# Kernel optimization log

Hardware: AMD Instinct MI355X
Metric: run time of the kernel (lower is better)

The kernel has to match this reference:

```python
import jax, jax.numpy as jnp
import numpy as np

B, T, EPROJS, DUNITS, ATT_DIM = 32, 2048, 512, 512, 512
ACONV_CHANS, ACONV_FILT = 32, 100
SCALING = 2.0


def _lin(k, fan_in, fan_out):
    k1, k2 = jax.random.split(k)
    lim = 1.0 / np.sqrt(fan_in)
    w = jax.random.uniform(k1, (fan_in, fan_out), minval=-lim, maxval=lim, dtype=jnp.float32)
    b = jax.random.uniform(k2, (fan_out,), minval=-lim, maxval=lim, dtype=jnp.float32)
    return w, b


def setup_inputs() -> dict:
    key = jax.random.key(0)
    ks = jax.random.split(key, 16)
    W_w, W_b = _lin(ks[0], DUNITS, ATT_DIM)
    V_w, V_b = _lin(ks[1], EPROJS, ATT_DIM)
    U_w, U_b = _lin(ks[2], DUNITS, ATT_DIM)
    g_w, g_b = _lin(ks[3], ATT_DIM, 1)
    K = 2 * ACONV_FILT + 1
    lim = 1.0 / np.sqrt(K)
    conv_w = jax.random.uniform(ks[4], (ACONV_CHANS, 1, K), minval=-lim, maxval=lim, dtype=jnp.float32)
    lim = 1.0 / np.sqrt(ATT_DIM)
    W_ih = jax.random.uniform(ks[5], (4 * ATT_DIM, ACONV_CHANS), minval=-lim, maxval=lim, dtype=jnp.float32)
    W_hh = jax.random.uniform(ks[6], (4 * ATT_DIM, ATT_DIM), minval=-lim, maxval=lim, dtype=jnp.float32)
    b_ih = jax.random.uniform(ks[7], (4 * ATT_DIM,), minval=-lim, maxval=lim, dtype=jnp.float32)
    b_hh = jax.random.uniform(ks[8], (4 * ATT_DIM,), minval=-lim, maxval=lim, dtype=jnp.float32)
    enc_hs_pad = jax.random.normal(ks[9], (B, T, EPROJS), dtype=jnp.float32)
    enc_hs_len = jax.random.randint(ks[10], (B,), T // 2, T + 1, dtype=jnp.int32)
    dec_z = jax.random.normal(ks[11], (B, DUNITS), dtype=jnp.float32)
    att_prev = jax.random.uniform(ks[12], (B, T), dtype=jnp.float32)
    att_h = jax.random.normal(ks[13], (B, ATT_DIM), dtype=jnp.float32)
    att_c = jax.random.normal(ks[14], (B, ATT_DIM), dtype=jnp.float32)
    return dict(enc_hs_pad=enc_hs_pad, enc_hs_len=enc_hs_len, dec_z=dec_z,
                att_prev=att_prev, att_h=att_h, att_c=att_c,
                W_w=W_w, W_b=W_b, V_w=V_w, V_b=V_b, U_w=U_w, U_b=U_b,
                g_w=g_w, g_b=g_b, conv_w=conv_w,
                W_ih=W_ih, W_hh=W_hh, b_ih=b_ih, b_hh=b_hh)


def reference(enc_hs_pad, enc_hs_len, dec_z, att_prev, att_h, att_c,
              W_w, W_b, V_w, V_b, U_w, U_b, g_w, g_b, conv_w,
              W_ih, W_hh, b_ih, b_hh):
    # pre-computed encoder projection: (B, T, att_dim)
    pre = jnp.einsum('bte,ea->bta', enc_hs_pad, V_w) + V_b
    # location conv over previous attention weights: (B, C, T)
    conv = jax.lax.conv_general_dilated(att_prev[:, None, :], conv_w,
                                        window_strides=(1,),
                                        padding=[(ACONV_FILT, ACONV_FILT)],
                                        dimension_numbers=('NCH', 'OIH', 'NCH'))
    feat = jnp.max(jax.nn.relu(conv), axis=-1)  # (B, C): max-pool over time
    # LSTMCell (torch gate order: i, f, g, o)
    gates = feat @ W_ih.T + b_ih + att_h @ W_hh.T + b_hh
    i, f, g, o = jnp.split(gates, 4, axis=-1)
    c_new = jax.nn.sigmoid(f) * att_c + jax.nn.sigmoid(i) * jnp.tanh(g)
    h_new = jax.nn.sigmoid(o) * jnp.tanh(c_new)
    # additive score
    dec_proj = dec_z @ U_w + U_b            # (B, att_dim)
    wh = h_new @ W_w + W_b                  # (B, att_dim)
    e = jnp.tanh(wh[:, None, :] + pre + dec_proj[:, None, :])  # (B, T, att_dim)
    score = jnp.einsum('bta,a->bt', e, g_w[:, 0]) + g_b[0]     # (B, T)
    mask = jnp.arange(T)[None, :] >= enc_hs_len[:, None]
    score = jnp.where(mask, jnp.asarray(-1e30, score.dtype), score)
    w = jax.nn.softmax(SCALING * score, axis=1)
    c_v = jnp.einsum('bte,bt->be', enc_hs_pad, w)  # (B, eprojs)
    return c_v, w, h_new, c_new
```

## Files before the change

kernel.cpp:

```cpp
#include <hip/hip_runtime.h>
#include <math.h>

#define BB 32
#define TT_SEQ 2048
#define EPROJS 512
#define ATT 512
#define NCH 32
#define FILT 100
#define KCONV 201
#define G4 2048

typedef unsigned short ushort_t;
typedef unsigned int uint_t;
typedef __attribute__((ext_vector_type(8))) short bf16x8_t;
typedef __attribute__((ext_vector_type(4))) float f32x4_t;

__device__ inline ushort_t f2bf(float f) {
    uint_t u = __float_as_uint(f);
    uint_t r = (u + 0x7fffu + ((u >> 16) & 1u)) >> 16;
    return (ushort_t)r;
}

__device__ inline float tanh_fast(float x) {
    float e = __expf(2.0f * x);
    return 1.0f - 2.0f / (e + 1.0f);
}

__global__ __launch_bounds__(256) void k_pre(const float* __restrict__ att_prev,
                                             const float* __restrict__ conv_w,
                                             float* __restrict__ feat,
                                             const float* __restrict__ vw,
                                             ushort_t* __restrict__ vwt,
                                             const float* __restrict__ U_b,
                                             const float* __restrict__ W_b,
                                             const float* __restrict__ V_b,
                                             float* __restrict__ add_vec) {
    __shared__ __align__(16) float shbuf[64 * 65];
    __shared__ float red[4];
    if (blockIdx.x < 1024) {
        int b = blockIdx.x >> 5;
        int c = blockIdx.x & 31;
        float* row = shbuf;
        for (int i = threadIdx.x; i < TT_SEQ + 2 * FILT + 8; i += 256) {
            int t = i - FILT;
            row[i] = (t >= 0 && t < TT_SEQ) ? att_prev[b * TT_SEQ + t] : 0.0f;
        }
        __syncthreads();
        const float* cw = conv_w + c * KCONV;
        int t0 = threadIdx.x * 8;
        float acc[8] = {0.f, 0.f, 0.f, 0.f, 0.f, 0.f, 0.f, 0.f};
        float4 r0 = *(const float4*)(row + t0);
        float4 r1 = *(const float4*)(row + t0 + 4);
        float r[8] = {r0.x, r0.y, r0.z, r0.w, r1.x, r1.y, r1.z, r1.w};
        for (int k = 0; k < 200; k += 8) {
            float4 n0 = *(const float4*)(row + t0 + k + 8);
            float4 n1 = *(const float4*)(row + t0 + k + 12);
            float nn[8] = {n0.x, n0.y, n0.z, n0.w, n1.x, n1.y, n1.z, n1.w};
            #pragma unroll
            for (int kk = 0; kk < 8; ++kk) {
                float w = cw[k + kk];
                #pragma unroll
                for (int i = 0; i < 8; ++i) {
                    float rv = (kk + i < 8) ? r[kk + i] : nn[kk + i - 8];
                    acc[i] = fmaf(w, rv, acc[i]);
                }
            }
            #pragma unroll
            for (int i = 0; i < 8; ++i) r[i] = nn[i];
        }
        float wlast = cw[200];
        #pragma unroll
        for (int i = 0; i < 8; ++i) acc[i] = fmaf(wlast, r[i], acc[i]);
        float m = 0.0f;
        #pragma unroll
        for (int i = 0; i < 8; ++i) m = fmaxf(m, acc[i]);
        #pragma unroll
        for (int off = 32; off; off >>= 1) m = fmaxf(m, __shfl_xor(m, off, 64));
        if ((threadIdx.x & 63) == 0) red[threadIdx.x >> 6] = m;
        __syncthreads();
        if (threadIdx.x == 0) {
            m = fmaxf(fmaxf(red[0], red[1]), fmaxf(red[2], red[3]));
            feat[b * NCH + c] = m;
        }
    } else {
        int id = blockIdx.x - 1024;
        int eb = (id & 7) * 64, ab = (id >> 3) * 64;
        float (*tile)[65] = (float (*)[65])shbuf;
        for (int it = 0; it < 16; ++it) {
            int idx = threadIdx.x + it * 256;
            int r = idx >> 6, c = idx & 63;
            tile[r][c] = vw[(size_t)(eb + r) * ATT + ab + c];
        }
        __syncthreads();
        for (int it = 0; it < 16; ++it) {
            int idx = threadIdx.x + it * 256;
            int r = idx >> 6, c = idx & 63;
            vwt[(size_t)(ab + r) * EPROJS + eb + c] = f2bf(tile[c][r]);
        }
        int i = id * 256 + threadIdx.x;
        int a = i & 511;
        add_vec[i] = U_b[a] + W_b[a] + V_b[a];
    }
}

#define HP 518
__global__ __launch_bounds__(256) void k_gates(const float* __restrict__ feat,
                                               const float* __restrict__ att_h,
                                               const float* __restrict__ W_ih,
                                               const float* __restrict__ W_hh,
                                               const float* __restrict__ b_ih,
                                               const float* __restrict__ b_hh,
                                               float* __restrict__ gates) {
    __shared__ float hsh[32 * HP];
    __shared__ float fsh[32 * 33];
    int tid = threadIdx.x;
    for (int i = tid; i < 32 * 512; i += 256) {
        int r = i >> 9, c = i & 511;
        hsh[r * HP + c] = att_h[i];
    }
    for (int i = tid; i < 1024; i += 256) fsh[(i >> 5) * 33 + (i & 31)] = feat[i];
    __syncthreads();
    int jl = tid >> 5, b = tid & 31;
    int j = blockIdx.x * 8 + jl;
    float acc = b_ih[j] + b_hh[j];
    const float4* wi = (const float4*)(W_ih + (size_t)j * NCH);
    #pragma unroll
    for (int k4 = 0; k4 < 8; ++k4) {
        float4 w = wi[k4];
        const float* f = fsh + b * 33 + k4 * 4;
        acc = fmaf(w.x, f[0], acc);
        acc = fmaf(w.y, f[1], acc);
        acc = fmaf(w.z, f[2], acc);
        acc = fmaf(w.w, f[3], acc);
    }
    const float4* wh = (const float4*)(W_hh + (size_t)j * ATT);
    float a0 = 0.f, a1 = 0.f, a2 = 0.f, a3 = 0.f;
    #pragma unroll 8
    for (int k4 = 0; k4 < 128; ++k4) {
        float4 w = wh[k4];
        float2 h0 = *(const float2*)(hsh + b * HP + k4 * 4);
        float2 h1 = *(const float2*)(hsh + b * HP + k4 * 4 + 2);
        a0 = fmaf(w.x, h0.x, a0);
        a1 = fmaf(w.y, h0.y, a1);
        a2 = fmaf(w.z, h1.x, a2);
        a3 = fmaf(w.w, h1.y, a3);
    }
    gates[(size_t)b * G4 + j] = acc + ((a0 + a1) + (a2 + a3));
}

__global__ __launch_bounds__(256) void k_hz(const float* __restrict__ gates,
                                            const float* __restrict__ att_c,
                                            const float* __restrict__ dec_z,
                                            const float* __restrict__ U_w,
                                            const float* __restrict__ W_w,
                                            float* __restrict__ h_out,
                                            float* __restrict__ c_out,
                                            float* __restrict__ add_vec) {
    int a0 = blockIdx.x * 32;
    int k0 = blockIdx.y * 64;
    __shared__ float zsh[32 * 65];
    __shared__ float hsh[32 * 65];
    __shared__ float us[64 * 33];
    __shared__ float ws2[64 * 33];
    int tid = threadIdx.x;
    for (int i = tid; i < 2048; i += 256) {
        int b = i >> 6, d = i & 63;
        int idx = b * ATT + k0 + d;
        const float* g = gates + (size_t)b * G4 + k0 + d;
        float ig = g[0], fg = g[ATT], gg = g[2 * ATT], og = g[3 * ATT];
        float si = 1.0f / (1.0f + expf(-ig));
        float sf = 1.0f / (1.0f + expf(-fg));
        float so = 1.0f / (1.0f + expf(-og));
        float cn = sf * att_c[idx] + si * tanhf(gg);
        float hn = so * tanhf(cn);
        hsh[b * 65 + d] = hn;
        if (blockIdx.x == 0) { c_out[idx] = cn; h_out[idx] = hn; }
        zsh[b * 65 + d] = dec_z[idx];
        int dr = i >> 5, c = i & 31;
        us[dr * 33 + c] = U_w[(size_t)(k0 + dr) * ATT + a0 + c];
        ws2[dr * 33 + c] = W_w[(size_t)(k0 + dr) * ATT + a0 + c];
    }
    __syncthreads();
    int al = tid >> 5, b = tid & 31;
    float acc[4] = {0.f, 0.f, 0.f, 0.f};
    for (int d = 0; d < 64; ++d) {
        float zv = zsh[b * 65 + d];
        float hv = hsh[b * 65 + d];
        #pragma unroll
        for (int m = 0; m < 4; ++m) {
            int a = al + 8 * m;
            acc[m] = fmaf(zv, us[d * 33 + a], acc[m]);
            acc[m] = fmaf(hv, ws2[d * 33 + a], acc[m]);
        }
    }
    #pragma unroll
    for (int m = 0; m < 4; ++m)
        atomicAdd(&add_vec[(size_t)b * ATT + a0 + al + 8 * m], acc[m]);
}

__global__ __launch_bounds__(512, 2) void k_gemm_score2(
        const float* __restrict__ enc,
        const ushort_t* __restrict__ Btbf,
        const float* __restrict__ add_vec,
        const float* __restrict__ g_w,
        const int* __restrict__ lens,
        float* __restrict__ score) {
    int mtile = blockIdx.x;
    int b = mtile >> 4;
    int t0 = (mtile & 15) * 128;
    if (t0 >= lens[b]) return;

    __shared__ __align__(16) ushort_t sA[128 * 64];
    __shared__ __align__(16) ushort_t sB[512 * 64];

    int tid = threadIdx.x;
    int lane = tid & 63;
    int wave = tid >> 6;
    int wm = wave >> 2, wn = wave & 3;
    int q = lane >> 4, l15 = lane & 15;

    const float* Ag = enc + (size_t)mtile * 128 * EPROJS;

    f32x4_t acc[4][8];
    #pragma unroll
    for (int i = 0; i < 4; ++i)
        #pragma unroll
        for (int j = 0; j < 8; ++j) acc[i][j] = (f32x4_t){0.f, 0.f, 0.f, 0.f};

    for (int kc = 0; kc < 8; ++kc) {
        __syncthreads();
        #pragma unroll
        for (int it = 0; it < 8; ++it) {
            int g = tid + it * 512;
            int n = g >> 3;
            int kq = g & 7;
            int kqs = kq ^ (n & 7);
            __builtin_amdgcn_global_load_lds(
                (const __attribute__((address_space(1))) void*)(Btbf + (size_t)n * EPROJS + kc * 64 + kqs * 8),
                (__attribute__((address_space(3))) void*)(sB + g * 8), 16, 0, 0);
        }
        #pragma unroll
        for (int it = 0; it < 2; ++it) {
            int g = tid + it * 512;
            int m = g >> 3;
            int kq = g & 7;
            int kqs = kq ^ (m & 7);
            const float* src = Ag + (size_t)m * EPROJS + kc * 64 + kqs * 8;
            float4 v0 = *(const float4*)(src);
            float4 v1 = *(const float4*)(src + 4);
            bf16x8_t o;
            o[0] = (short)f2bf(v0.x); o[1] = (short)f2bf(v0.y);
            o[2] = (short)f2bf(v0.z); o[3] = (short)f2bf(v0.w);
            o[4] = (short)f2bf(v1.x); o[5] = (short)f2bf(v1.y);
            o[6] = (short)f2bf(v1.z); o[7] = (short)f2bf(v1.w);
            *(bf16x8_t*)(sA + g * 8) = o;
        }
        __syncthreads();
        #pragma unroll
        for (int s = 0; s < 2; ++s) {
            bf16x8_t af[4], bfr[8];
            int kq = s * 4 + q;
            #pragma unroll
            for (int i = 0; i < 4; ++i) {
                int m = wm * 64 + i * 16 + l15;
                af[i] = *(const bf16x8_t*)(sA + (m * 8 + (kq ^ (m & 7))) * 8);
            }
            #pragma unroll
            for (int j = 0; j < 8; ++j) {
                int n = wn * 128 + j * 16 + l15;
                bfr[j] = *(const bf16x8_t*)(sB + (n * 8 + (kq ^ (n & 7))) * 8);
            }
            #pragma unroll
            for (int i = 0; i < 4; ++i)
                #pragma unroll
                for (int j = 0; j < 8; ++j)
                    acc[i][j] = __builtin_amdgcn_mfma_f32_16x16x32_bf16(af[i], bfr[j], acc[i][j], 0, 0, 0);
        }
    }

    float g8[8], av8[8];
    #pragma unroll
    for (int j = 0; j < 8; ++j) {
        int a = wn * 128 + j * 16 + l15;
        g8[j] = g_w[a];
        av8[j] = add_vec[b * ATT + a];
    }
    float s_ir[4][4];
    #pragma unroll
    for (int i = 0; i < 4; ++i) {
        #pragma unroll
        for (int r = 0; r < 4; ++r) {
            float s = 0.0f;
            #pragma unroll
            for (int j = 0; j < 8; ++j) {
                float x = acc[i][j][r] + av8[j];
                s = fmaf(g8[j], tanh_fast(x), s);
            }
            s_ir[i][r] = s;
        }
    }
    #pragma unroll
    for (int off = 8; off; off >>= 1) {
        #pragma unroll
        for (int i = 0; i < 4; ++i)
            #pragma unroll
            for (int r = 0; r < 4; ++r)
                s_ir[i][r] += __shfl_xor(s_ir[i][r], off, 16);
    }
    __syncthreads();
    float* sred = (float*)sA;
    if (tid < 128) sred[tid] = 0.0f;
    __syncthreads();
    if (l15 == 0) {
        #pragma unroll
        for (int i = 0; i < 4; ++i)
            #pragma unroll
            for (int r = 0; r < 4; ++r)
                atomicAdd(&sred[wm * 64 + i * 16 + q * 4 + r], s_ir[i][r]);
    }
    __syncthreads();
    if (tid < 128) score[b * TT_SEQ + t0 + tid] = sred[tid];
}

__global__ __launch_bounds__(256) void k_softmax(const float* __restrict__ score,
                                                 const int* __restrict__ lens,
                                                 float* __restrict__ w_out,
                                                 float* __restrict__ c_v) {
    int b = blockIdx.x;
    int len = lens[b];
    __shared__ float red[4];
    float vals[8];
    float m = -INFINITY;
    #pragma unroll
    for (int i = 0; i < 8; ++i) {
        int t = threadIdx.x + i * 256;
        float s = (t < len) ? 2.0f * score[b * TT_SEQ + t] : -INFINITY;
        vals[i] = s;
        m = fmaxf(m, s);
    }
    #pragma unroll
    for (int off = 32; off; off >>= 1) m = fmaxf(m, __shfl_xor(m, off, 64));
    if ((threadIdx.x & 63) == 0) red[threadIdx.x >> 6] = m;
    __syncthreads();
    m = fmaxf(fmaxf(red[0], red[1]), fmaxf(red[2], red[3]));
    __syncthreads();
    float sum = 0.0f;
    #pragma unroll
    for (int i = 0; i < 8; ++i) {
        float e = expf(vals[i] - m);
        vals[i] = e;
        sum += e;
    }
    #pragma unroll
    for (int off = 32; off; off >>= 1) sum += __shfl_xor(sum, off, 64);
    if ((threadIdx.x & 63) == 0) red[threadIdx.x >> 6] = sum;
    __syncthreads();
    sum = red[0] + red[1] + red[2] + red[3];
    float inv = 1.0f / sum;
    #pragma unroll
    for (int i = 0; i < 8; ++i) w_out[b * TT_SEQ + threadIdx.x + i * 256] = vals[i] * inv;
    for (int i = threadIdx.x; i < EPROJS; i += 256) c_v[b * EPROJS + i] = 0.0f;
}

__global__ __launch_bounds__(256) void k_ctx64(const float* __restrict__ enc,
                                               const float* __restrict__ w,
                                               const int* __restrict__ lens,
                                               float* __restrict__ c_v) {
    int b = blockIdx.y;
    int t0 = blockIdx.x * 64;
    if (t0 >= lens[b]) return;
    __shared__ float wsh[64];
    if (threadIdx.x < 64) wsh[threadIdx.x] = w[b * TT_SEQ + t0 + threadIdx.x];
    __syncthreads();
    const float* base = enc + ((size_t)b * TT_SEQ + t0) * EPROJS;
    float a0 = 0.f, a1 = 0.f;
    for (int t = 0; t < 64; ++t) {
        float wt = wsh[t];
        a0 = fmaf(wt, base[(size_t)t * EPROJS + threadIdx.x], a0);
        a1 = fmaf(wt, base[(size_t)t * EPROJS + threadIdx.x + 256], a1);
    }
    atomicAdd(&c_v[b * EPROJS + threadIdx.x], a0);
    atomicAdd(&c_v[b * EPROJS + threadIdx.x + 256], a1);
}

__global__ __launch_bounds__(256) void k_conv_fb(const float* __restrict__ att_prev,
                                                 const float* __restrict__ conv_w,
                                                 float* __restrict__ feat) {
    int b = blockIdx.x >> 5;
    int c = blockIdx.x & 31;
    __shared__ float row[TT_SEQ + 2 * FILT];
    __shared__ float wsh[KCONV];
    __shared__ float red[4];
    for (int i = threadIdx.x; i < TT_SEQ + 2 * FILT; i += 256) {
        int t = i - FILT;
        row[i] = (t >= 0 && t < TT_SEQ) ? att_prev[b * TT_SEQ + t] : 0.0f;
    }
    for (int i = threadIdx.x; i < KCONV; i += 256) wsh[i] = conv_w[c * KCONV + i];
    __syncthreads();
    float m = 0.0f;
    for (int t = threadIdx.x; t < TT_SEQ; t += 256) {
        float s = 0.0f;
        #pragma unroll 4
        for (int k = 0; k < KCONV; ++k) s = fmaf(wsh[k], row[t + k], s);
        m = fmaxf(m, s);
    }
    #pragma unroll
    for (int off = 32; off; off >>= 1) m = fmaxf(m, __shfl_xor(m, off, 64));
    if ((threadIdx.x & 63) == 0) red[threadIdx.x >> 6] = m;
    __syncthreads();
    if (threadIdx.x == 0) {
        m = fmaxf(fmaxf(red[0], red[1]), fmaxf(red[2], red[3]));
        feat[b * NCH + c] = m;
    }
}

__global__ __launch_bounds__(256) void k_lstm(const float* __restrict__ feat,
                                              const float* __restrict__ att_h,
                                              const float* __restrict__ att_c,
                                              const float* __restrict__ W_ih,
                                              const float* __restrict__ W_hh,
                                              const float* __restrict__ b_ih,
                                              const float* __restrict__ b_hh,
                                              float* __restrict__ h_out,
                                              float* __restrict__ c_out) {
    int b = blockIdx.x;
    __shared__ float fsh[NCH];
    __shared__ float hsh[ATT];
    __shared__ float gsh[G4];
    if (threadIdx.x < NCH) fsh[threadIdx.x] = feat[b * NCH + threadIdx.x];
    for (int i = threadIdx.x; i < ATT; i += 256) hsh[i] = att_h[b * ATT + i];
    __syncthreads();
    for (int j = threadIdx.x; j < G4; j += 256) {
        float acc = b_ih[j] + b_hh[j];
        const float* wi = W_ih + (size_t)j * NCH;
        #pragma unroll
        for (int c = 0; c < NCH; ++c) acc = fmaf(fsh[c], wi[c], acc);
        const float* wh = W_hh + (size_t)j * ATT;
        for (int a = 0; a < ATT; a += 4) {
            float4 w4 = *(const float4*)(wh + a);
            acc = fmaf(hsh[a + 0], w4.x, acc);
            acc = fmaf(hsh[a + 1], w4.y, acc);
            acc = fmaf(hsh[a + 2], w4.z, acc);
            acc = fmaf(hsh[a + 3], w4.w, acc);
        }
        gsh[j] = acc;
    }
    __syncthreads();
    for (int a = threadIdx.x; a < ATT; a += 256) {
        float ig = gsh[a], fg = gsh[ATT + a], gg = gsh[2 * ATT + a], og = gsh[3 * ATT + a];
        float si = 1.0f / (1.0f + expf(-ig));
        float sf = 1.0f / (1.0f + expf(-fg));
        float so = 1.0f / (1.0f + expf(-og));
        float cn = sf * att_c[b * ATT + a] + si * tanhf(gg);
        float hn = so * tanhf(cn);
        c_out[b * ATT + a] = cn;
        h_out[b * ATT + a] = hn;
    }
}

__global__ __launch_bounds__(256) void k_addvec(const float* __restrict__ dec_z,
                                                const float* __restrict__ h_new,
                                                const float* __restrict__ U_w,
                                                const float* __restrict__ U_b,
                                                const float* __restrict__ W_w,
                                                const float* __restrict__ W_b,
                                                const float* __restrict__ V_b,
                                                float* __restrict__ add_vec) {
    int b = blockIdx.x;
    __shared__ float zsh[ATT];
    __shared__ float hsh[ATT];
    for (int i = threadIdx.x; i < ATT; i += 256) {
        zsh[i] = dec_z[b * ATT + i];
        hsh[i] = h_new[b * ATT + i];
    }
    __syncthreads();
    for (int a = threadIdx.x; a < ATT; a += 256) {
        float acc = U_b[a] + W_b[a] + V_b[a];
        for (int d = 0; d < ATT; ++d) {
            acc = fmaf(zsh[d], U_w[(size_t)d * ATT + a], acc);
            acc = fmaf(hsh[d], W_w[(size_t)d * ATT + a], acc);
        }
        add_vec[b * ATT + a] = acc;
    }
}

#define TTILE 16
#define SR 516
__global__ __launch_bounds__(256) void k_score(const float* __restrict__ enc,
                                               const float* __restrict__ V_w,
                                               const float* __restrict__ add_vec,
                                               const float* __restrict__ g_w,
                                               const float* __restrict__ g_b,
                                               const int* __restrict__ lens,
                                               float* __restrict__ score) {
    int b = blockIdx.y;
    int t0 = blockIdx.x * TTILE;
    int len = lens[b];
    if (t0 >= len) return;
    __shared__ float enc_t[TTILE * SR];
    __shared__ float ash[ATT];
    __shared__ float gwsh[ATT];
    const float* src = enc + ((size_t)b * TT_SEQ + t0) * EPROJS;
    for (int i = threadIdx.x; i < TTILE * 128; i += 256) {
        int r = i >> 7, c4 = (i & 127) << 2;
        *(float4*)(enc_t + r * SR + c4) = *(const float4*)(src + (size_t)r * EPROJS + c4);
    }
    for (int i = threadIdx.x; i < ATT; i += 256) {
        ash[i] = add_vec[b * ATT + i];
        gwsh[i] = g_w[i];
    }
    __syncthreads();
    int t = threadIdx.x >> 4;
    int al = threadIdx.x & 15;
    const float* er = enc_t + t * SR;
    float sc = 0.0f;
    #pragma unroll
    for (int c = 0; c < 2; ++c) {
        float4 acc0 = {0, 0, 0, 0}, acc1 = {0, 0, 0, 0}, acc2 = {0, 0, 0, 0}, acc3 = {0, 0, 0, 0};
        int abase = c * 256 + al * 4;
        const float* vp = V_w + abase;
        for (int e = 0; e < EPROJS; ++e) {
            float s = er[e];
            const float* rowp = vp + (size_t)e * ATT;
            float4 w0 = *(const float4*)(rowp);
            float4 w1 = *(const float4*)(rowp + 64);
            float4 w2 = *(const float4*)(rowp + 128);
            float4 w3 = *(const float4*)(rowp + 192);
            acc0.x = fmaf(s, w0.x, acc0.x); acc0.y = fmaf(s, w0.y, acc0.y);
            acc0.z = fmaf(s, w0.z, acc0.z); acc0.w = fmaf(s, w0.w, acc0.w);
            acc1.x = fmaf(s, w1.x, acc1.x); acc1.y = fmaf(s, w1.y, acc1.y);
            acc1.z = fmaf(s, w1.z, acc1.z); acc1.w = fmaf(s, w1.w, acc1.w);
            acc2.x = fmaf(s, w2.x, acc2.x); acc2.y = fmaf(s, w2.y, acc2.y);
            acc2.z = fmaf(s, w2.z, acc2.z); acc2.w = fmaf(s, w2.w, acc2.w);
            acc3.x = fmaf(s, w3.x, acc3.x); acc3.y = fmaf(s, w3.y, acc3.y);
            acc3.z = fmaf(s, w3.z, acc3.z); acc3.w = fmaf(s, w3.w, acc3.w);
        }
        float av[16] = {acc0.x, acc0.y, acc0.z, acc0.w,
                        acc1.x, acc1.y, acc1.z, acc1.w,
                        acc2.x, acc2.y, acc2.z, acc2.w,
                        acc3.x, acc3.y, acc3.z, acc3.w};
        #pragma unroll
        for (int k = 0; k < 16; ++k) {
            int a = abase + (k >> 2) * 64 + (k & 3);
            sc = fmaf(gwsh[a], tanhf(av[k] + ash[a]), sc);
        }
    }
    #pragma unroll
    for (int off = 8; off; off >>= 1) sc += __shfl_xor(sc, off, 16);
    if (al == 0) score[b * TT_SEQ + t0 + t] = sc + g_b[0];
}

extern "C" void kernel_launch(void* const* d_in, const int* in_sizes, int n_in,
                              void* d_out, int out_size, void* d_ws, size_t ws_size,
                              hipStream_t stream) {
    const float* enc      = (const float*)d_in[0];
    const int*   lens     = (const int*)d_in[1];
    const float* dec_z    = (const float*)d_in[2];
    const float* att_prev = (const float*)d_in[3];
    const float* att_h    = (const float*)d_in[4];
    const float* att_c    = (const float*)d_in[5];
    const float* W_w      = (const float*)d_in[6];
    const float* W_b      = (const float*)d_in[7];
    const float* V_w      = (const float*)d_in[8];
    const float* V_b      = (const float*)d_in[9];
    const float* U_w      = (const float*)d_in[10];
    const float* U_b      = (const float*)d_in[11];
    const float* g_w      = (const float*)d_in[12];
    const float* g_b      = (const float*)d_in[13];
    const float* conv_w   = (const float*)d_in[14];
    const float* W_ih     = (const float*)d_in[15];
    const float* W_hh     = (const float*)d_in[16];
    const float* b_ih     = (const float*)d_in[17];
    const float* b_hh     = (const float*)d_in[18];

    float* out   = (float*)d_out;
    float* c_v   = out;
    float* w_out = out + BB * EPROJS;
    float* h_out = w_out + BB * TT_SEQ;
    float* c_out = h_out + BB * ATT;

    const size_t need = (size_t)ATT * EPROJS * 2 +
                        (size_t)(1024 + BB * ATT + BB * TT_SEQ + BB * G4) * sizeof(float);

    if (ws_size >= need) {
        ushort_t* vwt  = (ushort_t*)d_ws;
        float* feat    = (float*)(vwt + (size_t)ATT * EPROJS);
        float* add_vec = feat + 1024;
        float* score   = add_vec + BB * ATT;
        float* gates   = score + BB * TT_SEQ;

        k_pre<<<dim3(1024 + 64), dim3(256), 0, stream>>>(att_prev, conv_w, feat,
                                                         V_w, vwt, U_b, W_b, V_b, add_vec);
        k_gates<<<dim3(G4 / 8), dim3(256), 0, stream>>>(feat, att_h, W_ih, W_hh,
                                                        b_ih, b_hh, gates);
        k_hz<<<dim3(16, 8), dim3(256), 0, stream>>>(gates, att_c, dec_z, U_w, W_w,
                                                    h_out, c_out, add_vec);
        k_gemm_score2<<<dim3(512), dim3(512), 0, stream>>>(enc, vwt, add_vec, g_w,
                                                           lens, score);
        k_softmax<<<dim3(BB), dim3(256), 0, stream>>>(score, lens, w_out, c_v);
        k_ctx64<<<dim3(32, BB), dim3(256), 0, stream>>>(enc, w_out, lens, c_v);
    } else {
        float* ws      = (float*)d_ws;
        float* feat    = ws;
        float* add_vec = ws + 1024;
        float* score   = ws + 1024 + BB * ATT;

        k_conv_fb<<<dim3(BB * NCH), dim3(256), 0, stream>>>(att_prev, conv_w, feat);
        k_lstm<<<dim3(BB), dim3(256), 0, stream>>>(feat, att_h, att_c, W_ih, W_hh,
                                                   b_ih, b_hh, h_out, c_out);
        k_addvec<<<dim3(BB), dim3(256), 0, stream>>>(dec_z, h_out, U_w, U_b, W_w, W_b,
                                                     V_b, add_vec);
        k_score<<<dim3(TT_SEQ / TTILE, BB), dim3(256), 0, stream>>>(enc, V_w, add_vec,
                                                                    g_w, g_b, lens, score);
        k_softmax<<<dim3(BB), dim3(256), 0, stream>>>(score, lens, w_out, c_v);
        k_ctx64<<<dim3(32, BB), dim3(256), 0, stream>>>(enc, w_out, lens, c_v);
    }
}
```

Before: 326.5 us.

## Split score GEMM across attention-dim tiles and reduce scores atomically

```diff
diff --git a/kernel.cpp b/kernel.cpp
--- a/kernel.cpp
+++ b/kernel.cpp
@@ -34,7 +34,8 @@
                                              const float* __restrict__ U_b,
                                              const float* __restrict__ W_b,
                                              const float* __restrict__ V_b,
-                                             float* __restrict__ add_vec) {
+                                             float* __restrict__ add_vec,
+                                             float* __restrict__ score) {
     __shared__ __align__(16) float shbuf[64 * 65];
     __shared__ float red[4];
     if (blockIdx.x < 1024) {
@@ -100,6 +101,7 @@
         int i = id * 256 + threadIdx.x;
         int a = i & 511;
         add_vec[i] = U_b[a] + W_b[a] + V_b[a];
+        ((float4*)score)[id * 256 + threadIdx.x] = (float4){0.f, 0.f, 0.f, 0.f};
     }
 }
 
@@ -198,7 +200,7 @@
         atomicAdd(&add_vec[(size_t)b * ATT + a0 + al + 8 * m], acc[m]);
 }
 
-__global__ __launch_bounds__(512, 2) void k_gemm_score2(
+__global__ __launch_bounds__(256) void k_gemm_score3(
         const float* __restrict__ enc,
         const ushort_t* __restrict__ Btbf,
         const float* __restrict__ add_vec,
@@ -209,39 +211,44 @@
     int b = mtile >> 4;
     int t0 = (mtile & 15) * 128;
     if (t0 >= lens[b]) return;
+    int n0 = blockIdx.y * 128;
 
     __shared__ __align__(16) ushort_t sA[128 * 64];
-    __shared__ __align__(16) ushort_t sB[512 * 64];
+    __shared__ __align__(16) ushort_t sB[128 * 64];
+    __shared__ float sred[128];
 
     int tid = threadIdx.x;
     int lane = tid & 63;
     int wave = tid >> 6;
-    int wm = wave >> 2, wn = wave & 3;
+    int wm = wave >> 1, wn = wave & 1;
     int q = lane >> 4, l15 = lane & 15;
 
+    if (tid < 128) sred[tid] = 0.0f;
+
     const float* Ag = enc + (size_t)mtile * 128 * EPROJS;
-
-    f32x4_t acc[4][8];
+    const ushort_t* Bg = Btbf + (size_t)n0 * EPROJS;
+
+    f32x4_t acc[4][4];
     #pragma unroll
     for (int i = 0; i < 4; ++i)
         #pragma unroll
-        for (int j = 0; j < 8; ++j) acc[i][j] = (f32x4_t){0.f, 0.f, 0.f, 0.f};
+        for (int j = 0; j < 4; ++j) acc[i][j] = (f32x4_t){0.f, 0.f, 0.f, 0.f};
 
     for (int kc = 0; kc < 8; ++kc) {
         __syncthreads();
         #pragma unroll
-        for (int it = 0; it < 8; ++it) {
-            int g = tid + it * 512;
+        for (int it = 0; it < 4; ++it) {
+            int g = tid + it * 256;
             int n = g >> 3;
             int kq = g & 7;
             int kqs = kq ^ (n & 7);
             __builtin_amdgcn_global_load_lds(
-                (const __attribute__((address_space(1))) void*)(Btbf + (size_t)n * EPROJS + kc * 64 + kqs * 8),
+                (const __attribute__((address_space(1))) void*)(Bg + (size_t)n * EPROJS + kc * 64 + kqs * 8),
                 (__attribute__((address_space(3))) void*)(sB + g * 8), 16, 0, 0);
         }
         #pragma unroll
-        for (int it = 0; it < 2; ++it) {
-            int g = tid + it * 512;
+        for (int it = 0; it < 4; ++it) {
+            int g = tid + it * 256;
             int m = g >> 3;
             int kq = g & 7;
             int kqs = kq ^ (m & 7);
@@ -258,7 +265,7 @@
         __syncthreads();
         #pragma unroll
         for (int s = 0; s < 2; ++s) {
-            bf16x8_t af[4], bfr[8];
+            bf16x8_t af[4], bfr[4];
             int kq = s * 4 + q;
             #pragma unroll
             for (int i = 0; i < 4; ++i) {
@@ -266,24 +273,24 @@
                 af[i] = *(const bf16x8_t*)(sA + (m * 8 + (kq ^ (m & 7))) * 8);
             }
             #pragma unroll
-            for (int j = 0; j < 8; ++j) {
-                int n = wn * 128 + j * 16 + l15;
+            for (int j = 0; j < 4; ++j) {
+                int n = wn * 64 + j * 16 + l15;
                 bfr[j] = *(const bf16x8_t*)(sB + (n * 8 + (kq ^ (n & 7))) * 8);
             }
             #pragma unroll
             for (int i = 0; i < 4; ++i)
                 #pragma unroll
-                for (int j = 0; j < 8; ++j)
+                for (int j = 0; j < 4; ++j)
                     acc[i][j] = __builtin_amdgcn_mfma_f32_16x16x32_bf16(af[i], bfr[j], acc[i][j], 0, 0, 0);
         }
     }
 
-    float g8[8], av8[8];
-    #pragma unroll
-    for (int j = 0; j < 8; ++j) {
-        int a = wn * 128 + j * 16 + l15;
-        g8[j] = g_w[a];
-        av8[j] = add_vec[b * ATT + a];
+    float g4[4], av4[4];
+    #pragma unroll
+    for (int j = 0; j < 4; ++j) {
+        int a = n0 + wn * 64 + j * 16 + l15;
+        g4[j] = g_w[a];
+        av4[j] = add_vec[b * ATT + a];
     }
     float s_ir[4][4];
     #pragma unroll
@@ -292,9 +299,9 @@
         for (int r = 0; r < 4; ++r) {
             float s = 0.0f;
             #pragma unroll
-            for (int j = 0; j < 8; ++j) {
-                float x = acc[i][j][r] + av8[j];
-                s = fmaf(g8[j], tanh_fast(x), s);
+            for (int j = 0; j < 4; ++j) {
+                float x = acc[i][j][r] + av4[j];
+                s = fmaf(g4[j], tanh_fast(x), s);
             }
             s_ir[i][r] = s;
         }
@@ -307,10 +314,6 @@
             for (int r = 0; r < 4; ++r)
                 s_ir[i][r] += __shfl_xor(s_ir[i][r], off, 16);
     }
-    __syncthreads();
-    float* sred = (float*)sA;
-    if (tid < 128) sred[tid] = 0.0f;
-    __syncthreads();
     if (l15 == 0) {
         #pragma unroll
         for (int i = 0; i < 4; ++i)
@@ -319,7 +322,7 @@
                 atomicAdd(&sred[wm * 64 + i * 16 + q * 4 + r], s_ir[i][r]);
     }
     __syncthreads();
-    if (tid < 128) score[b * TT_SEQ + t0 + tid] = sred[tid];
+    if (tid < 128) atomicAdd(&score[b * TT_SEQ + t0 + tid], sred[tid]);
 }
 
 __global__ __launch_bounds__(256) void k_softmax(const float* __restrict__ score,
@@ -590,13 +593,14 @@
         float* gates   = score + BB * TT_SEQ;
 
         k_pre<<<dim3(1024 + 64), dim3(256), 0, stream>>>(att_prev, conv_w, feat,
-                                                         V_w, vwt, U_b, W_b, V_b, add_vec);
+                                                         V_w, vwt, U_b, W_b, V_b,
+                                                         add_vec, score);
         k_gates<<<dim3(G4 / 8), dim3(256), 0, stream>>>(feat, att_h, W_ih, W_hh,
                                                         b_ih, b_hh, gates);
         k_hz<<<dim3(16, 8), dim3(256), 0, stream>>>(gates, att_c, dec_z, U_w, W_w,
                                                     h_out, c_out, add_vec);
-        k_gemm_score2<<<dim3(512), dim3(512), 0, stream>>>(enc, vwt, add_vec, g_w,
-                                                           lens, score);
+        k_gemm_score3<<<dim3(512, 4), dim3(256), 0, stream>>>(enc, vwt, add_vec, g_w,
+                                                              lens, score);
         k_softmax<<<dim3(BB), dim3(256), 0, stream>>>(score, lens, w_out, c_v);
         k_ctx64<<<dim3(32, BB), dim3(256), 0, stream>>>(enc, w_out, lens, c_v);
     } else {
```

New measurement: 358.3 us. 1.1x slower.
